# Optimization experiments

Measured on AMD Instinct MI355X. Metric: run time of the kernel, lower is better.

## Reference

```python
import jax, jax.numpy as jnp
import numpy as np

B, C, D, H, W = 2, 512, 32, 32, 32
L, CTX = 256, 768
NH, HD, G = 8, 64, 8
EPS = 1e-5


def group_norm(x, w, b):
    Bb, Cc, Dd, Hh, Ww = x.shape
    xg = x.reshape(Bb, G, Cc // G, Dd, Hh, Ww)
    mu = xg.mean(axis=(2, 3, 4, 5), keepdims=True)
    var = xg.var(axis=(2, 3, 4, 5), keepdims=True)
    xn = ((xg - mu) * jax.lax.rsqrt(var + EPS)).reshape(Bb, Cc, Dd, Hh, Ww)
    return xn * w[None, :, None, None, None] + b[None, :, None, None, None]


def layer_norm(x, w, b):
    mu = x.mean(axis=-1, keepdims=True)
    var = x.var(axis=-1, keepdims=True)
    return (x - mu) * jax.lax.rsqrt(var + EPS) * w + b


def setup_inputs() -> dict:
    key = jax.random.key(0)
    ks = jax.random.split(key, 8)
    s = 0.02  # weight init scale
    return {
        "x": jax.random.normal(ks[0], (B, C, D, H, W), jnp.float32),
        "context": jax.random.normal(ks[1], (B, L, CTX), jnp.float32),
        "gn_w": jnp.ones((C,), jnp.float32),
        "gn_b": jnp.zeros((C,), jnp.float32),
        "ln_w": jnp.ones((CTX,), jnp.float32),
        "ln_b": jnp.zeros((CTX,), jnp.float32),
        "q_w": jax.random.normal(ks[2], (C, C), jnp.float32) * s,
        "q_b": jnp.zeros((C,), jnp.float32),
        "k_w": jax.random.normal(ks[3], (C, CTX), jnp.float32) * s,
        "k_b": jnp.zeros((C,), jnp.float32),
        "v_w": jax.random.normal(ks[4], (C, CTX), jnp.float32) * s,
        "v_b": jnp.zeros((C,), jnp.float32),
        "proj_w": jax.random.normal(ks[5], (C, C), jnp.float32) * s,
        "proj_b": jnp.zeros((C,), jnp.float32),
    }


def reference(x, context, gn_w, gn_b, ln_w, ln_b, q_w, q_b, k_w, k_b, v_w, v_b, proj_w, proj_b):
    Bb, Cc, Dd, Hh, Ww = x.shape
    S = Dd * Hh * Ww
    h = group_norm(x, gn_w, gn_b)
    ctx = layer_norm(context, ln_w, ln_b)
    # 1x1 Conv3d == per-voxel linear over channels
    q = jnp.einsum('oc,bcdhw->bodhw', q_w, h) + q_b[None, :, None, None, None]
    q = q.reshape(Bb, NH, HD, S)                                        # (b,h,e,s)
    k = (ctx @ k_w.T + k_b).reshape(Bb, L, NH, HD).transpose(0, 2, 1, 3)  # (b,h,l,e)
    v = (ctx @ v_w.T + v_b).reshape(Bb, L, NH, HD).transpose(0, 2, 1, 3)  # (b,h,l,e)
    scale = HD ** -0.5
    attn = jnp.einsum('bhes,bhle->bhsl', q, k) * scale                  # (b,h,S,L)
    attn = jax.nn.softmax(attn, axis=-1)
    out = jnp.einsum('bhsl,bhle->bhes', attn, v).reshape(Bb, Cc, Dd, Hh, Ww)
    out = jnp.einsum('oc,bcdhw->bodhw', proj_w, out) + proj_b[None, :, None, None, None]
    return out + x
```

## Files before the change

### kernel.cpp

```cpp
#include <hip/hip_runtime.h>

typedef unsigned short u16;
typedef __attribute__((ext_vector_type(4))) float f32x4;
typedef __attribute__((ext_vector_type(8))) short bf16x8;
typedef __attribute__((ext_vector_type(8))) u16 u16x8;
typedef __attribute__((ext_vector_type(4))) u16 u16x4;

#define DEVI __device__ __forceinline__

constexpr int C_ = 512, S_ = 32768, L_ = 256, CTX_ = 768;

DEVI u16 f2b(float f) {
    union { float f; unsigned u; } x; x.f = f;
    unsigned r = x.u + 0x7fffu + ((x.u >> 16) & 1u);
    return (u16)(r >> 16);
}

DEVI f32x4 mfma16(bf16x8 a, bf16x8 b, f32x4 c) {
    return __builtin_amdgcn_mfma_f32_16x16x32_bf16(a, b, c, 0, 0, 0);
}

DEVI void gload16(const void* g, void* l) {
    __builtin_amdgcn_global_load_lds(
        (const __attribute__((address_space(1))) void*)g,
        (__attribute__((address_space(3))) void*)l, 16, 0, 0);
}

__global__ __launch_bounds__(256) void cvt_w(
    const float* __restrict__ a0, const float* __restrict__ a1,
    const float* __restrict__ a2, const float* __restrict__ a3,
    u16* __restrict__ o0, u16* __restrict__ o1,
    u16* __restrict__ o2, u16* __restrict__ o3)
{
    int which = blockIdx.y;
    const float* src = which == 0 ? a0 : which == 1 ? a1 : which == 2 ? a2 : a3;
    u16* dst = which == 0 ? o0 : which == 1 ? o1 : which == 2 ? o2 : o3;
    int n4 = (which == 1 || which == 2) ? (512 * 768 / 4) : (512 * 512 / 4);
    int i = blockIdx.x * 256 + threadIdx.x;
    if (i < n4) {
        float4 v = ((const float4*)src)[i];
        u16x4 o; o[0] = f2b(v.x); o[1] = f2b(v.y); o[2] = f2b(v.z); o[3] = f2b(v.w);
        ((u16x4*)dst)[i] = o;
    }
}

__global__ __launch_bounds__(256) void gn_partial(const float* __restrict__ x,
                                                  float* __restrict__ part)
{
    const int bg = blockIdx.y, blk = blockIdx.x, tid = threadIdx.x;
    const float* base = x + (size_t)bg * 64 * S_ + (size_t)blk * 512;
    float s1 = 0.f, s2 = 0.f;
    for (int c = 0; c < 64; ++c) {
        const float* row = base + (size_t)c * S_;
        float v0 = row[tid], v1 = row[tid + 256];
        s1 += v0 + v1; s2 += v0 * v0 + v1 * v1;
    }
    for (int m = 1; m < 64; m <<= 1) { s1 += __shfl_xor(s1, m); s2 += __shfl_xor(s2, m); }
    __shared__ float a1[4], a2[4];
    int w = tid >> 6, lane = tid & 63;
    if (lane == 0) { a1[w] = s1; a2[w] = s2; }
    __syncthreads();
    if (tid == 0) {
        part[(bg * 64 + blk) * 2 + 0] = a1[0] + a1[1] + a1[2] + a1[3];
        part[(bg * 64 + blk) * 2 + 1] = a2[0] + a2[1] + a2[2] + a2[3];
    }
}

__global__ __launch_bounds__(64) void gn_final(const float* __restrict__ part,
                                               float* __restrict__ stats)
{
    int bg = blockIdx.x, tid = threadIdx.x;
    float s1 = part[(bg * 64 + tid) * 2], s2 = part[(bg * 64 + tid) * 2 + 1];
    for (int m = 1; m < 64; m <<= 1) { s1 += __shfl_xor(s1, m); s2 += __shfl_xor(s2, m); }
    if (tid == 0) {
        const float invN = 1.0f / (64.0f * (float)S_);
        float mu = s1 * invN, var = s2 * invN - mu * mu;
        stats[bg * 2] = mu;
        stats[bg * 2 + 1] = rsqrtf(var + 1e-5f);
    }
}

__global__ __launch_bounds__(256) void gn_apply(
    const float* __restrict__ x, const float* __restrict__ stats,
    const float* __restrict__ gw, const float* __restrict__ gb,
    u16* __restrict__ ht)
{
    __shared__ float tile[64][65];
    const int tid = threadIdx.x, sl = tid & 63, c4 = tid >> 6;
    const int s0 = blockIdx.x * 64, c0 = blockIdx.y * 64, b = blockIdx.z;
    const int bg = b * 8 + (c0 >> 6);
    const float mu = stats[bg * 2], rstd = stats[bg * 2 + 1];
#pragma unroll
    for (int i = 0; i < 16; ++i) {
        int cl = c4 * 16 + i;
        float wv = gw[c0 + cl], bv = gb[c0 + cl];
        float v = x[((size_t)(b * C_ + c0 + cl)) * S_ + s0 + sl];
        tile[sl][cl] = (v - mu) * rstd * wv + bv;
    }
    __syncthreads();
#pragma unroll
    for (int i = 0; i < 16; ++i) {
        int so = c4 * 16 + i;
        ht[((size_t)(b * S_ + s0 + so)) * C_ + c0 + sl] = f2b(tile[so][sl]);
    }
}

__global__ __launch_bounds__(256) void ln_ctx(
    const float* __restrict__ ctx, const float* __restrict__ lw,
    const float* __restrict__ lb, u16* __restrict__ cn)
{
    const int row = blockIdx.x, tid = threadIdx.x;
    const float* p = ctx + (size_t)row * CTX_;
    float v0 = p[tid], v1 = p[tid + 256], v2 = p[tid + 512];
    float s1 = v0 + v1 + v2, s2 = v0 * v0 + v1 * v1 + v2 * v2;
    for (int m = 1; m < 64; m <<= 1) { s1 += __shfl_xor(s1, m); s2 += __shfl_xor(s2, m); }
    __shared__ float a1[4], a2[4];
    int w = tid >> 6, lane = tid & 63;
    if (lane == 0) { a1[w] = s1; a2[w] = s2; }
    __syncthreads();
    s1 = a1[0] + a1[1] + a1[2] + a1[3];
    s2 = a2[0] + a2[1] + a2[2] + a2[3];
    const float invN = 1.0f / 768.0f;
    float mu = s1 * invN, rstd = rsqrtf(s2 * invN - mu * mu + 1e-5f);
    u16* o = cn + (size_t)row * CTX_;
    o[tid]       = f2b((v0 - mu) * rstd * lw[tid]       + lb[tid]);
    o[tid + 256] = f2b((v1 - mu) * rstd * lw[tid + 256] + lb[tid + 256]);
    o[tid + 512] = f2b((v2 - mu) * rstd * lw[tid + 512] + lb[tid + 512]);
}

template <int MODE>
__global__ __launch_bounds__(256, 2) void gemm_nt(
    const u16* __restrict__ A, const u16* __restrict__ Bp,
    const float* __restrict__ bias, void* __restrict__ outp,
    const float* __restrict__ resid, int K, int ldo,
    size_t aStride, size_t bStride, size_t oStride, float scale)
{
    __shared__ __align__(16) u16 lA[128 * 32];
    __shared__ __align__(16) u16 lB[128 * 32];
    const int tid = threadIdx.x;
    const int w = tid >> 6, lane = tid & 63;
    const int g = lane >> 4, r = lane & 15;
    const int m0 = blockIdx.x * 128, n0 = blockIdx.y * 128;
    const int z = blockIdx.z;
    A += (size_t)z * aStride;
    Bp += (size_t)z * bStride;

    const int srow = w * 32 + (lane >> 2);
    const int skc = (lane & 3) * 8;
    const int wr = w >> 1, wc = w & 1;

    f32x4 acc[4][4];
#pragma unroll
    for (int m = 0; m < 4; ++m)
#pragma unroll
        for (int n = 0; n < 4; ++n) acc[m][n] = f32x4{0.f, 0.f, 0.f, 0.f};

    for (int kt = 0; kt < K; kt += 32) {
        __syncthreads();
#pragma unroll
        for (int j = 0; j < 2; ++j) {
            int row = srow + j * 16;
            gload16(A + (size_t)(m0 + row) * K + kt + skc, &lA[(w * 32 + j * 16) * 32]);
            gload16(Bp + (size_t)(n0 + row) * K + kt + skc, &lB[(w * 32 + j * 16) * 32]);
        }
        __syncthreads();
        bf16x8 af[4], bf_[4];
#pragma unroll
        for (int m = 0; m < 4; ++m) af[m] = *(const bf16x8*)&lA[(wr * 64 + m * 16 + r) * 32 + g * 8];
#pragma unroll
        for (int n = 0; n < 4; ++n) bf_[n] = *(const bf16x8*)&lB[(wc * 64 + n * 16 + r) * 32 + g * 8];
#pragma unroll
        for (int m = 0; m < 4; ++m)
#pragma unroll
            for (int n = 0; n < 4; ++n)
                acc[m][n] = mfma16(af[m], bf_[n], acc[m][n]);
    }

    if constexpr (MODE == 0) {
        u16* ob = (u16*)outp + (size_t)z * oStride;
#pragma unroll
        for (int n = 0; n < 4; ++n) {
            int gn = n0 + wc * 64 + n * 16 + r;
            float bn = bias[gn] * scale;
#pragma unroll
            for (int m = 0; m < 4; ++m) {
                int gm = m0 + wr * 64 + m * 16 + g * 4;
#pragma unroll
                for (int i = 0; i < 4; ++i)
                    ob[(size_t)(gm + i) * ldo + gn] = f2b(acc[m][n][i] * scale + bn);
            }
        }
    } else if constexpr (MODE == 1) {
        u16* ob = (u16*)outp;
#pragma unroll
        for (int n = 0; n < 4; ++n) {
            int gn = n0 + wc * 64 + n * 16 + r;
            float bn = bias[gn];
#pragma unroll
            for (int m = 0; m < 4; ++m) {
                int gm = m0 + wr * 64 + m * 16 + g * 4;
                int bb = gm >> 8, l = gm & 255;
                u16x4 pk;
#pragma unroll
                for (int i = 0; i < 4; ++i) pk[i] = f2b(acc[m][n][i] + bn);
                *(u16x4*)&ob[((size_t)(bb * 512 + gn)) * 256 + l] = pk;
            }
        }
    } else {
        float* of = (float*)outp + (size_t)z * oStride;
        const float* rs = resid + (size_t)z * oStride;
#pragma unroll
        for (int m = 0; m < 4; ++m) {
            int gm = m0 + wr * 64 + m * 16 + g * 4;
#pragma unroll
            for (int i = 0; i < 4; ++i) {
                float bm = bias[gm + i];
#pragma unroll
                for (int n = 0; n < 4; ++n) {
                    int gn = n0 + wc * 64 + n * 16 + r;
                    size_t idx = (size_t)(gm + i) * ldo + gn;
                    of[idx] = acc[m][n][i] + bm + rs[idx];
                }
            }
        }
    }
}

__global__ __launch_bounds__(256, 2) void attn_kernel(
    const u16* __restrict__ q, const u16* __restrict__ kk,
    const u16* __restrict__ vv, u16* __restrict__ ao)
{
    __shared__ __align__(16) u16 sm[32768];
    const int tid = threadIdx.x;
    const int w = tid >> 6, lane = tid & 63;
    const int g = lane >> 4, r = lane & 15;
    const int bh = blockIdx.y, b = bh >> 3, h = bh & 7;
    const int s0 = blockIdx.x * 128;

    {
        const u16* kbase = kk + ((size_t)b * L_) * C_ + h * 64;
#pragma unroll
        for (int j = 0; j < 8; ++j) {
            int idx = j * 256 + tid;
            int l = idx >> 3, ch = idx & 7;
            u16x8 val = *(const u16x8*)(kbase + (size_t)l * C_ + ch * 8);
            *(u16x8*)&sm[l * 64 + ((ch ^ (l & 7)) << 3)] = val;
        }
        const u16* vbase = vv + ((size_t)bh * 64) * 256;
#pragma unroll
        for (int j = 0; j < 8; ++j) {
            int idx = j * 256 + tid;
            int e = idx >> 5, ch = idx & 31;
            u16x8 val = *(const u16x8*)(vbase + (size_t)e * 256 + ch * 8);
            *(u16x8*)&sm[16384 + e * 256 + ((ch ^ (e & 7)) << 3)] = val;
        }
    }
    __syncthreads();

    const int sw = s0 + w * 32;
    bf16x8 qf[2][2];
#pragma unroll
    for (int m = 0; m < 2; ++m)
#pragma unroll
        for (int kt = 0; kt < 2; ++kt)
            qf[m][kt] = *(const bf16x8*)(q + ((size_t)(b * S_ + sw + m * 16 + r)) * C_
                                         + h * 64 + kt * 32 + g * 8);

    f32x4 accs[2][16];
#pragma unroll
    for (int m = 0; m < 2; ++m)
#pragma unroll
        for (int n = 0; n < 16; ++n) accs[m][n] = f32x4{0.f, 0.f, 0.f, 0.f};
#pragma unroll
    for (int n = 0; n < 16; ++n) {
#pragma unroll
        for (int kt = 0; kt < 2; ++kt) {
            int c = kt * 4 + g;
            bf16x8 kf = *(const bf16x8*)&sm[(n * 16 + r) * 64 + ((c ^ (r & 7)) << 3)];
#pragma unroll
            for (int m = 0; m < 2; ++m) accs[m][n] = mfma16(qf[m][kt], kf, accs[m][n]);
        }
    }

    float mx[2][4], inv[2][4];
#pragma unroll
    for (int m = 0; m < 2; ++m)
#pragma unroll
        for (int i = 0; i < 4; ++i) {
            float v = accs[m][0][i];
#pragma unroll
            for (int n = 1; n < 16; ++n) v = fmaxf(v, accs[m][n][i]);
#pragma unroll
            for (int msk = 1; msk < 16; msk <<= 1) v = fmaxf(v, __shfl_xor(v, msk));
            mx[m][i] = v;
        }
#pragma unroll
    for (int m = 0; m < 2; ++m)
#pragma unroll
        for (int i = 0; i < 4; ++i) {
            float sum = 0.f;
#pragma unroll
            for (int n = 0; n < 16; ++n) {
                float e = __expf(accs[m][n][i] - mx[m][i]);
                accs[m][n][i] = e; sum += e;
            }
#pragma unroll
            for (int msk = 1; msk < 16; msk <<= 1) sum += __shfl_xor(sum, msk);
            inv[m][i] = 1.0f / sum;
        }

    __syncthreads();

    f32x4 acco[2][4];
#pragma unroll
    for (int m = 0; m < 2; ++m)
#pragma unroll
        for (int n = 0; n < 4; ++n) acco[m][n] = f32x4{0.f, 0.f, 0.f, 0.f};

#pragma unroll
    for (int half = 0; half < 2; ++half) {
#pragma unroll
        for (int m = 0; m < 2; ++m)
#pragma unroll
            for (int n8 = 0; n8 < 8; ++n8) {
                int n = half * 8 + n8;
                int lh = n8 * 16 + r;
#pragma unroll
                for (int i = 0; i < 4; ++i) {
                    int sl = m * 16 + g * 4 + i;
                    float p = accs[m][n][i] * inv[m][i];
                    sm[w * 4096 + sl * 128 + (((lh >> 3) ^ (sl & 7)) << 3) + (lh & 7)] = f2b(p);
                }
            }
#pragma unroll
        for (int kt = 0; kt < 4; ++kt) {
            int l0 = kt * 32 + g * 8;
            int lg = half * 128 + l0;
            bf16x8 pf[2], vf[4];
#pragma unroll
            for (int m = 0; m < 2; ++m) {
                int sl = m * 16 + r;
                pf[m] = *(const bf16x8*)&sm[w * 4096 + sl * 128 + (((l0 >> 3) ^ (r & 7)) << 3)];
            }
#pragma unroll
            for (int n = 0; n < 4; ++n) {
                int e = n * 16 + r;
                vf[n] = *(const bf16x8*)&sm[16384 + e * 256 + (((lg >> 3) ^ (r & 7)) << 3)];
            }
#pragma unroll
            for (int m = 0; m < 2; ++m)
#pragma unroll
                for (int n = 0; n < 4; ++n)
                    acco[m][n] = mfma16(pf[m], vf[n], acco[m][n]);
        }
    }

#pragma unroll
    for (int m = 0; m < 2; ++m)
#pragma unroll
        for (int n = 0; n < 4; ++n)
#pragma unroll
            for (int i = 0; i < 4; ++i) {
                int s = sw + m * 16 + g * 4 + i;
                int e = n * 16 + r;
                ao[((size_t)(b * S_ + s)) * C_ + h * 64 + e] = f2b(acco[m][n][i]);
            }
}

extern "C" void kernel_launch(void* const* d_in, const int* in_sizes, int n_in,
                              void* d_out, int out_size, void* d_ws, size_t ws_size,
                              hipStream_t stream)
{
    (void)in_sizes; (void)n_in; (void)out_size; (void)ws_size;
    const float* x    = (const float*)d_in[0];
    const float* ctx  = (const float*)d_in[1];
    const float* gn_w = (const float*)d_in[2];
    const float* gn_b = (const float*)d_in[3];
    const float* ln_w = (const float*)d_in[4];
    const float* ln_b = (const float*)d_in[5];
    const float* q_w  = (const float*)d_in[6];
    const float* q_b  = (const float*)d_in[7];
    const float* k_w  = (const float*)d_in[8];
    const float* k_b  = (const float*)d_in[9];
    const float* v_w  = (const float*)d_in[10];
    const float* v_b  = (const float*)d_in[11];
    const float* p_w  = (const float*)d_in[12];
    const float* p_b  = (const float*)d_in[13];
    float* out = (float*)d_out;

    char* ws = (char*)d_ws;
    constexpr size_t WS_WQ   = 0;
    constexpr size_t WS_WK   = WS_WQ + (size_t)512 * 512 * 2;
    constexpr size_t WS_WV   = WS_WK + (size_t)512 * 768 * 2;
    constexpr size_t WS_WP   = WS_WV + (size_t)512 * 768 * 2;
    constexpr size_t WS_PART = WS_WP + (size_t)512 * 512 * 2;
    constexpr size_t WS_STAT = WS_PART + (size_t)16 * 64 * 2 * 4;
    constexpr size_t WS_CTXN = WS_STAT + 256;
    constexpr size_t WS_K    = WS_CTXN + (size_t)512 * 768 * 2;
    constexpr size_t WS_V    = WS_K + (size_t)2 * 8 * 256 * 64 * 2;
    constexpr size_t WS_Q    = WS_V + (size_t)2 * 8 * 256 * 64 * 2;
    constexpr size_t WS_H    = WS_Q + (size_t)2 * 32768 * 512 * 2;

    u16* wq = (u16*)(ws + WS_WQ);
    u16* wk = (u16*)(ws + WS_WK);
    u16* wv = (u16*)(ws + WS_WV);
    u16* wp = (u16*)(ws + WS_WP);
    float* part  = (float*)(ws + WS_PART);
    float* stats = (float*)(ws + WS_STAT);
    u16* ctxn = (u16*)(ws + WS_CTXN);
    u16* kt   = (u16*)(ws + WS_K);
    u16* vt   = (u16*)(ws + WS_V);
    u16* qt   = (u16*)(ws + WS_Q);
    u16* ht   = (u16*)(ws + WS_H);
    u16* ao   = ht;

    const size_t bsc = (size_t)S_ * C_;

    cvt_w<<<dim3(384, 4), 256, 0, stream>>>(q_w, k_w, v_w, p_w, wq, wk, wv, wp);
    gn_partial<<<dim3(64, 16), 256, 0, stream>>>(x, part);
    gn_final<<<16, 64, 0, stream>>>(part, stats);
    gn_apply<<<dim3(512, 8, 2), 256, 0, stream>>>(x, stats, gn_w, gn_b, ht);
    ln_ctx<<<512, 256, 0, stream>>>(ctx, ln_w, ln_b, ctxn);
    gemm_nt<0><<<dim3(256, 4, 2), 256, 0, stream>>>(ht, wq, q_b, qt, nullptr,
                                                    512, 512, bsc, 0, bsc, 0.125f);
    gemm_nt<0><<<dim3(4, 4, 1), 256, 0, stream>>>(ctxn, wk, k_b, kt, nullptr,
                                                  768, 512, 0, 0, 0, 1.0f);
    gemm_nt<1><<<dim3(4, 4, 1), 256, 0, stream>>>(ctxn, wv, v_b, vt, nullptr,
                                                  768, 0, 0, 0, 0, 1.0f);
    attn_kernel<<<dim3(256, 16), 256, 0, stream>>>(qt, kt, vt, ao);
    gemm_nt<2><<<dim3(4, 256, 2), 256, 0, stream>>>(wp, ao, p_b, out, x,
                                                    512, S_, 0, bsc, bsc, 1.0f);
}
```

Measured before the change: 330.5 us.

## Keep softmax probabilities in registers via transposed QK MFMA and permlane swaps

```diff
diff --git a/kernel.cpp b/kernel.cpp
--- a/kernel.cpp
+++ b/kernel.cpp
@@ -1,10 +1,12 @@
 #include <hip/hip_runtime.h>
 
 typedef unsigned short u16;
+typedef unsigned int u32;
 typedef __attribute__((ext_vector_type(4))) float f32x4;
 typedef __attribute__((ext_vector_type(8))) short bf16x8;
 typedef __attribute__((ext_vector_type(8))) u16 u16x8;
 typedef __attribute__((ext_vector_type(4))) u16 u16x4;
+typedef __attribute__((ext_vector_type(4))) u32 u32x4;
 
 #define DEVI __device__ __forceinline__
 
@@ -24,6 +26,18 @@
     __builtin_amdgcn_global_load_lds(
         (const __attribute__((address_space(1))) void*)g,
         (__attribute__((address_space(3))) void*)l, 16, 0, 0);
+}
+
+DEVI u32 cvtpk(float lo, float hi) {
+    u32 d;
+    asm("v_cvt_pk_bf16_f32 %0, %1, %2" : "=v"(d) : "v"(lo), "v"(hi));
+    return d;
+}
+DEVI void pl32(u32& a, u32& b) {
+    asm volatile("v_permlane32_swap_b32 %0, %1" : "+v"(a), "+v"(b));
+}
+DEVI void pl16(u32& a, u32& b) {
+    asm volatile("v_permlane16_swap_b32 %0, %1" : "+v"(a), "+v"(b));
 }
 
 __global__ __launch_bounds__(256) void cvt_w(
@@ -255,7 +269,6 @@
             *(u16x8*)&sm[16384 + e * 256 + ((ch ^ (e & 7)) << 3)] = val;
         }
     }
-    __syncthreads();
 
     const int sw = s0 + w * 32;
     bf16x8 qf[2][2];
@@ -265,12 +278,14 @@
         for (int kt = 0; kt < 2; ++kt)
             qf[m][kt] = *(const bf16x8*)(q + ((size_t)(b * S_ + sw + m * 16 + r)) * C_
                                          + h * 64 + kt * 32 + g * 8);
+    __syncthreads();
 
     f32x4 accs[2][16];
 #pragma unroll
     for (int m = 0; m < 2; ++m)
 #pragma unroll
         for (int n = 0; n < 16; ++n) accs[m][n] = f32x4{0.f, 0.f, 0.f, 0.f};
+    __builtin_amdgcn_s_setprio(1);
 #pragma unroll
     for (int n = 0; n < 16; ++n) {
 #pragma unroll
@@ -278,38 +293,33 @@
             int c = kt * 4 + g;
             bf16x8 kf = *(const bf16x8*)&sm[(n * 16 + r) * 64 + ((c ^ (r & 7)) << 3)];
 #pragma unroll
-            for (int m = 0; m < 2; ++m) accs[m][n] = mfma16(qf[m][kt], kf, accs[m][n]);
-        }
-    }
-
-    float mx[2][4], inv[2][4];
-#pragma unroll
-    for (int m = 0; m < 2; ++m)
-#pragma unroll
-        for (int i = 0; i < 4; ++i) {
-            float v = accs[m][0][i];
-#pragma unroll
-            for (int n = 1; n < 16; ++n) v = fmaxf(v, accs[m][n][i]);
-#pragma unroll
-            for (int msk = 1; msk < 16; msk <<= 1) v = fmaxf(v, __shfl_xor(v, msk));
-            mx[m][i] = v;
-        }
-#pragma unroll
-    for (int m = 0; m < 2; ++m)
-#pragma unroll
-        for (int i = 0; i < 4; ++i) {
-            float sum = 0.f;
-#pragma unroll
-            for (int n = 0; n < 16; ++n) {
-                float e = __expf(accs[m][n][i] - mx[m][i]);
+            for (int m = 0; m < 2; ++m) accs[m][n] = mfma16(kf, qf[m][kt], accs[m][n]);
+        }
+    }
+    __builtin_amdgcn_s_setprio(0);
+
+    float inv[2];
+#pragma unroll
+    for (int m = 0; m < 2; ++m) {
+        float mx = accs[m][0][0];
+#pragma unroll
+        for (int n = 0; n < 16; ++n)
+#pragma unroll
+            for (int i = 0; i < 4; ++i) mx = fmaxf(mx, accs[m][n][i]);
+        mx = fmaxf(mx, __shfl_xor(mx, 16));
+        mx = fmaxf(mx, __shfl_xor(mx, 32));
+        float sum = 0.f;
+#pragma unroll
+        for (int n = 0; n < 16; ++n)
+#pragma unroll
+            for (int i = 0; i < 4; ++i) {
+                float e = __expf(accs[m][n][i] - mx);
                 accs[m][n][i] = e; sum += e;
             }
-#pragma unroll
-            for (int msk = 1; msk < 16; msk <<= 1) sum += __shfl_xor(sum, msk);
-            inv[m][i] = 1.0f / sum;
-        }
-
-    __syncthreads();
+        sum += __shfl_xor(sum, 16);
+        sum += __shfl_xor(sum, 32);
+        inv[m] = 1.0f / sum;
+    }
 
     f32x4 acco[2][4];
 #pragma unroll
@@ -318,41 +328,34 @@
         for (int n = 0; n < 4; ++n) acco[m][n] = f32x4{0.f, 0.f, 0.f, 0.f};
 
 #pragma unroll
-    for (int half = 0; half < 2; ++half) {
+    for (int c = 0; c < 8; ++c) {
+        bf16x8 pa[2];
+#pragma unroll
+        for (int m = 0; m < 2; ++m) {
+            u32 x0 = cvtpk(accs[m][2 * c][0] * inv[m], accs[m][2 * c][1] * inv[m]);
+            u32 x1 = cvtpk(accs[m][2 * c][2] * inv[m], accs[m][2 * c][3] * inv[m]);
+            u32 y0 = cvtpk(accs[m][2 * c + 1][0] * inv[m], accs[m][2 * c + 1][1] * inv[m]);
+            u32 y1 = cvtpk(accs[m][2 * c + 1][2] * inv[m], accs[m][2 * c + 1][3] * inv[m]);
+            pl32(x0, y0);
+            pl32(x1, y1);
+            pl16(x0, y0);
+            pl16(x1, y1);
+            u32x4 pw; pw[0] = x0; pw[1] = x1; pw[2] = y0; pw[3] = y1;
+            pa[m] = *(bf16x8*)&pw;
+        }
+        bf16x8 vf[4];
+#pragma unroll
+        for (int n = 0; n < 4; ++n) {
+            int e = n * 16 + r;
+            vf[n] = *(const bf16x8*)&sm[16384 + e * 256 + (((c * 4 + g) ^ (r & 7)) << 3)];
+        }
+        __builtin_amdgcn_s_setprio(1);
 #pragma unroll
         for (int m = 0; m < 2; ++m)
 #pragma unroll
-            for (int n8 = 0; n8 < 8; ++n8) {
-                int n = half * 8 + n8;
-                int lh = n8 * 16 + r;
-#pragma unroll
-                for (int i = 0; i < 4; ++i) {
-                    int sl = m * 16 + g * 4 + i;
-                    float p = accs[m][n][i] * inv[m][i];
-                    sm[w * 4096 + sl * 128 + (((lh >> 3) ^ (sl & 7)) << 3) + (lh & 7)] = f2b(p);
-                }
-            }
-#pragma unroll
-        for (int kt = 0; kt < 4; ++kt) {
-            int l0 = kt * 32 + g * 8;
-            int lg = half * 128 + l0;
-            bf16x8 pf[2], vf[4];
-#pragma unroll
-            for (int m = 0; m < 2; ++m) {
-                int sl = m * 16 + r;
-                pf[m] = *(const bf16x8*)&sm[w * 4096 + sl * 128 + (((l0 >> 3) ^ (r & 7)) << 3)];
-            }
-#pragma unroll
-            for (int n = 0; n < 4; ++n) {
-                int e = n * 16 + r;
-                vf[n] = *(const bf16x8*)&sm[16384 + e * 256 + (((lg >> 3) ^ (r & 7)) << 3)];
-            }
-#pragma unroll
-            for (int m = 0; m < 2; ++m)
-#pragma unroll
-                for (int n = 0; n < 4; ++n)
-                    acco[m][n] = mfma16(pf[m], vf[n], acco[m][n]);
-        }
+            for (int n = 0; n < 4; ++n)
+                acco[m][n] = mfma16(pa[m], vf[n], acco[m][n]);
+        __builtin_amdgcn_s_setprio(0);
     }
 
 #pragma unroll
```

Result: faster. 307.8 us (-6.9%).
